# Performance work log

Measured on AMD Instinct MI355X. Metric: run time of the kernel, lower is better.

The kernel has to match this reference:

```python
import jax, jax.numpy as jnp
import numpy as np

N = 100000   # nodes
E = 1600000  # edges
F = 128      # in = out features
BN_EPS = 1e-5


def setup_inputs() -> dict:
    key = jax.random.key(0)
    ks = jax.random.split(key, 20)
    s = 1.0 / np.sqrt(F)
    inp = {
        "x": jax.random.normal(ks[0], (N, F), dtype=jnp.float32),
        "edge_index": jax.random.randint(ks[1], (2, E), 0, N, dtype=jnp.int64),
        "edge_type": jax.random.randint(ks[2], (E,), 0, 2, dtype=jnp.int64),
        # self-loop linear
        "w_sl": jax.random.normal(ks[3], (F, F), dtype=jnp.float32) * s,
        "b_sl": jnp.zeros((F,), dtype=jnp.float32),
        # GIN MLP for relation 0 (edge_type==0)
        "w1_n": jax.random.normal(ks[4], (F, F), dtype=jnp.float32) * s,
        "b1_n": jnp.zeros((F,), dtype=jnp.float32),
        "gamma_n": jnp.ones((F,), dtype=jnp.float32),
        "beta_n": jnp.zeros((F,), dtype=jnp.float32),
        "w2_n": jax.random.normal(ks[5], (F, F), dtype=jnp.float32) * s,
        "b2_n": jnp.zeros((F,), dtype=jnp.float32),
        # GIN MLP for relation 1 (edge_type==1)
        "w1_d": jax.random.normal(ks[6], (F, F), dtype=jnp.float32) * s,
        "b1_d": jnp.zeros((F,), dtype=jnp.float32),
        "gamma_d": jnp.ones((F,), dtype=jnp.float32),
        "beta_d": jnp.zeros((F,), dtype=jnp.float32),
        "w2_d": jax.random.normal(ks[7], (F, F), dtype=jnp.float32) * s,
        "b2_d": jnp.zeros((F,), dtype=jnp.float32),
        # gate linear: 3F -> F
        "w_gat": jax.random.normal(ks[8], (F, 3 * F), dtype=jnp.float32) * (1.0 / np.sqrt(3 * F)),
        "b_gat": jnp.zeros((F,), dtype=jnp.float32),
    }
    return inp


def _gin_branch(x, src, dst, mask, w1, b1, gamma, beta, w2, b2):
    # masked gather-scatter: equivalent to selecting edge columns with edge_type==r
    msg = x[src] * mask[:, None]                         # [E, F]
    agg = jax.ops.segment_sum(msg, dst, num_segments=N)  # [N, F]
    h = agg + x                                          # (1 + eps)*x with eps=0
    h = h @ w1.T + b1
    # BatchNorm1d, training-mode batch statistics (biased variance)
    mu = jnp.mean(h, axis=0)
    var = jnp.var(h, axis=0)
    h = gamma * (h - mu) * jax.lax.rsqrt(var + BN_EPS) + beta
    h = jax.nn.relu(h)
    return h @ w2.T + b2


def reference(x, edge_index, edge_type, w_sl, b_sl,
              w1_n, b1_n, gamma_n, beta_n, w2_n, b2_n,
              w1_d, b1_d, gamma_d, beta_d, w2_d, b2_d,
              w_gat, b_gat):
    src, dst = edge_index[0], edge_index[1]
    mask_n = (edge_type == 0).astype(x.dtype)
    mask_d = (edge_type == 1).astype(x.dtype)

    x_new_x = x @ w_sl.T + b_sl
    x_new_n = _gin_branch(x, src, dst, mask_n, w1_n, b1_n, gamma_n, beta_n, w2_n, b2_n)
    x_new_d = _gin_branch(x, src, dst, mask_d, w1_d, b1_d, gamma_d, beta_d, w2_d, b2_d)

    cat = jnp.concatenate((x_new_x, x_new_n, x_new_d), axis=1)   # [N, 3F]
    gat_raw = jax.nn.softmax(cat @ w_gat.T + b_gat, axis=-1)     # [N, F]
    gat = jnp.cumsum(gat_raw, axis=-1)
    out = (x_new_x + x_new_n) * (1.0 - gat) + (x_new_x + x_new_n + jnp.flip(x_new_d, axis=1)) * gat
    return out
```

## Files before the change

kernel.cpp:

```cpp
#include <hip/hip_runtime.h>
#include <stdint.h>

#define FF 128
#define MFMA __builtin_amdgcn_mfma_f32_16x16x32_bf16

typedef __attribute__((ext_vector_type(8))) short bf8_t;
typedef __attribute__((ext_vector_type(4))) float f4_t;
typedef __attribute__((ext_vector_type(8))) uint16_t us8_t;

__device__ __forceinline__ uint16_t f2bf(float f) {
  union { float f; uint32_t u; } v; v.f = f;
  return (uint16_t)((v.u + 0x7fffu + ((v.u >> 16) & 1u)) >> 16);
}
__device__ __forceinline__ float bf2f(uint16_t h) {
  union { uint32_t u; float f; } v; v.u = ((uint32_t)h) << 16;
  return v.f;
}

#define STAGE_W8(Wp, rsb, cb)                                                  \
  do {                                                                         \
    uint4 tmp_[4];                                                             \
    _Pragma("unroll") for (int j_ = 0; j_ < 4; ++j_) {                         \
      int k_ = j_ * 8 + w;                                                     \
      int r_ = ((k_ & 1) << 6) + lane;                                         \
      int c_ = k_ >> 1;                                                        \
      tmp_[j_] = *(const uint4*)((const char*)(Wp) + (size_t)r_ * (rsb) +      \
                                 (cb) + c_ * 16);                              \
    }                                                                          \
    _Pragma("unroll") for (int j_ = 0; j_ < 4; ++j_) {                         \
      int k_ = j_ * 8 + w;                                                     \
      *(uint4*)((char*)wlds + k_ * 1024 + lane * 16) = tmp_[j_];               \
    }                                                                          \
  } while (0)

__global__ __launch_bounds__(256) void cvt_w_k(
    const float* __restrict__ wsl, const float* __restrict__ w1n,
    const float* __restrict__ w2n, const float* __restrict__ w1d,
    const float* __restrict__ w2d, const float* __restrict__ wgat,
    uint16_t* __restrict__ o) {
  int i = blockIdx.x * 256 + threadIdx.x;
  const int NW = 5 * 16384;
  if (i >= NW + 49152) return;
  float v;
  if (i < NW) {
    int wsel = i >> 14, j = i & 16383;
    const float* p = (wsel == 0) ? wsl : (wsel == 1) ? w1n : (wsel == 2) ? w2n
                     : (wsel == 3) ? w1d : w2d;
    v = p[j];
  } else {
    v = wgat[i - NW];
  }
  o[i] = f2bf(v);
}

__global__ __launch_bounds__(256) void cvt_x_k(const float* __restrict__ x,
                                               uint16_t* __restrict__ xb, int n4) {
  int i = blockIdx.x * 256 + threadIdx.x;
  if (i >= n4) return;
  float4 v = ((const float4*)x)[i];
  uint2 o;
  o.x = ((uint32_t)f2bf(v.y) << 16) | f2bf(v.x);
  o.y = ((uint32_t)f2bf(v.w) << 16) | f2bf(v.z);
  ((uint2*)xb)[i] = o;
}

__global__ __launch_bounds__(256) void hist_k(const int* __restrict__ dst,
                                              const int* __restrict__ ety,
                                              int* __restrict__ hist, int E) {
  int i = blockIdx.x * 256 + threadIdx.x;
  if (i < E) atomicAdd(&hist[(dst[i] << 1) | ety[i]], 1);
}

__global__ __launch_bounds__(256) void scan1_k(const int* __restrict__ hist,
                                               int* __restrict__ off,
                                               int* __restrict__ bsum, int nbins) {
  int i = blockIdx.x * 256 + threadIdx.x;
  int v = (i < nbins) ? hist[i] : 0;
  int lane = threadIdx.x & 63, w = threadIdx.x >> 6;
  int s = v;
#pragma unroll
  for (int d = 1; d < 64; d <<= 1) {
    int o = __shfl_up(s, (unsigned)d, 64);
    if (lane >= d) s += o;
  }
  __shared__ int wsum[4];
  if (lane == 63) wsum[w] = s;
  __syncthreads();
  int add = 0;
  for (int k = 0; k < w; ++k) add += wsum[k];
  s += add;
  if (i < nbins) off[i] = s - v;
  if (threadIdx.x == 255) bsum[blockIdx.x] = s;
}

__global__ __launch_bounds__(1024) void scan2_k(int* __restrict__ bsum, int nb) {
  int t = threadIdx.x;
  int v = (t < nb) ? bsum[t] : 0;
  int lane = t & 63, w = t >> 6;
  int s = v;
#pragma unroll
  for (int d = 1; d < 64; d <<= 1) {
    int o = __shfl_up(s, (unsigned)d, 64);
    if (lane >= d) s += o;
  }
  __shared__ int ws[16];
  if (lane == 63) ws[w] = s;
  __syncthreads();
  int add = 0;
  for (int k = 0; k < w; ++k) add += ws[k];
  s += add;
  if (t < nb) bsum[t] = s - v;
}

__global__ __launch_bounds__(256) void scan3_k(int* __restrict__ off,
                                               int* __restrict__ ccur,
                                               const int* __restrict__ bsum,
                                               int nbins, int E) {
  int i = blockIdx.x * 256 + threadIdx.x;
  if (i < nbins) {
    int v = off[i] + bsum[blockIdx.x];
    off[i] = v;
    if ((i & 511) == 0) ccur[i >> 9] = v;
  }
  if (i == nbins) off[i] = E;
}

#define BK_EPT 16
__global__ __launch_bounds__(256) void bucketize_k(const int* __restrict__ src,
                                                   const int* __restrict__ dst,
                                                   const int* __restrict__ ety,
                                                   int* __restrict__ ccur,
                                                   uint32_t* __restrict__ bk,
                                                   int E, int nbuckets) {
  __shared__ int lhist[512];
  __shared__ int lbase[512];
  const int tid = threadIdx.x;
  const int base = blockIdx.x * (256 * BK_EPT);
  for (int j = tid; j < nbuckets; j += 256) lhist[j] = 0;
  __syncthreads();

  uint32_t pk[BK_EPT];
  uint32_t rk[BK_EPT];
#pragma unroll
  for (int j = 0; j < BK_EPT; ++j) {
    int i = base + j * 256 + tid;
    if (i < E) {
      int bin = (dst[i] << 1) | ety[i];
      int bucket = bin >> 9;
      int rank = atomicAdd(&lhist[bucket], 1);
      pk[j] = (uint32_t)src[i] | ((uint32_t)(bin & 511) << 17);
      rk[j] = (uint32_t)bucket | ((uint32_t)rank << 9);
    } else {
      rk[j] = 0xFFFFFFFFu;
    }
  }
  __syncthreads();
  for (int j = tid; j < nbuckets; j += 256) {
    int c = lhist[j];
    lbase[j] = c ? atomicAdd(&ccur[j], c) : 0;
  }
  __syncthreads();
#pragma unroll
  for (int j = 0; j < BK_EPT; ++j) {
    if (rk[j] != 0xFFFFFFFFu) {
      int bucket = (int)(rk[j] & 511u);
      int rank = (int)(rk[j] >> 9);
      bk[lbase[bucket] + rank] = pk[j];
    }
  }
}

__global__ __launch_bounds__(256) void sctfine_k(const int* __restrict__ off,
                                                 const uint32_t* __restrict__ bk,
                                                 int* __restrict__ ssrc, int nbins) {
  __shared__ int lcur[512];
  const int b = blockIdx.x;
  const int binbase = b << 9;
  const int binend = min(binbase + 512, nbins);
  for (int j = threadIdx.x; j < binend - binbase; j += 256)
    lcur[j] = off[binbase + j];
  __syncthreads();
  const int estart = off[binbase], eend = off[binend];
  for (int i = estart + (int)threadIdx.x; i < eend; i += 256) {
    uint32_t pk = bk[i];
    int pos = atomicAdd(&lcur[pk >> 17], 1);
    ssrc[pos] = (int)(pk & 0x1FFFFu);
  }
}

__global__ __launch_bounds__(256) void agg_k(const int* __restrict__ off,
                                             const int* __restrict__ ssrc,
                                             const uint16_t* __restrict__ xb,
                                             const float* __restrict__ x,
                                             uint16_t* __restrict__ xanb,
                                             uint16_t* __restrict__ xadb, int nbins) {
  int wid = (blockIdx.x * 256 + threadIdx.x) >> 6;
  int lane = threadIdx.x & 63;
  if (wid >= nbins) return;
  int e = off[wid], end = off[wid + 1];
  float ax = 0.f, ay = 0.f, bx = 0.f, by = 0.f;
  for (; e + 7 < end; e += 8) {
    uint32_t v0 = ((const uint32_t*)(xb + (size_t)ssrc[e] * FF))[lane];
    uint32_t v1 = ((const uint32_t*)(xb + (size_t)ssrc[e + 1] * FF))[lane];
    uint32_t v2 = ((const uint32_t*)(xb + (size_t)ssrc[e + 2] * FF))[lane];
    uint32_t v3 = ((const uint32_t*)(xb + (size_t)ssrc[e + 3] * FF))[lane];
    uint32_t v4 = ((const uint32_t*)(xb + (size_t)ssrc[e + 4] * FF))[lane];
    uint32_t v5 = ((const uint32_t*)(xb + (size_t)ssrc[e + 5] * FF))[lane];
    uint32_t v6 = ((const uint32_t*)(xb + (size_t)ssrc[e + 6] * FF))[lane];
    uint32_t v7 = ((const uint32_t*)(xb + (size_t)ssrc[e + 7] * FF))[lane];
    ax += bf2f((uint16_t)(v0 & 0xffffu)) + bf2f((uint16_t)(v2 & 0xffffu)) +
          bf2f((uint16_t)(v4 & 0xffffu)) + bf2f((uint16_t)(v6 & 0xffffu));
    ay += bf2f((uint16_t)(v0 >> 16)) + bf2f((uint16_t)(v2 >> 16)) +
          bf2f((uint16_t)(v4 >> 16)) + bf2f((uint16_t)(v6 >> 16));
    bx += bf2f((uint16_t)(v1 & 0xffffu)) + bf2f((uint16_t)(v3 & 0xffffu)) +
          bf2f((uint16_t)(v5 & 0xffffu)) + bf2f((uint16_t)(v7 & 0xffffu));
    by += bf2f((uint16_t)(v1 >> 16)) + bf2f((uint16_t)(v3 >> 16)) +
          bf2f((uint16_t)(v5 >> 16)) + bf2f((uint16_t)(v7 >> 16));
  }
  for (; e + 1 < end; e += 2) {
    uint32_t v0 = ((const uint32_t*)(xb + (size_t)ssrc[e] * FF))[lane];
    uint32_t v1 = ((const uint32_t*)(xb + (size_t)ssrc[e + 1] * FF))[lane];
    ax += bf2f((uint16_t)(v0 & 0xffffu));
    ay += bf2f((uint16_t)(v0 >> 16));
    bx += bf2f((uint16_t)(v1 & 0xffffu));
    by += bf2f((uint16_t)(v1 >> 16));
  }
  if (e < end) {
    uint32_t v0 = ((const uint32_t*)(xb + (size_t)ssrc[e] * FF))[lane];
    ax += bf2f((uint16_t)(v0 & 0xffffu));
    ay += bf2f((uint16_t)(v0 >> 16));
  }
  ax += bx;
  ay += by;
  int n = wid >> 1;
  float2 xo = ((const float2*)(x + (size_t)n * FF))[lane];
  ax += xo.x;
  ay += xo.y;
  uint32_t o = ((uint32_t)f2bf(ay) << 16) | f2bf(ax);
  uint16_t* dstp = (wid & 1) ? xadb : xanb;
  ((uint32_t*)(dstp + (size_t)n * FF))[lane] = o;
}

__global__ __launch_bounds__(512) void gemm1_k(
    const uint16_t* __restrict__ xanb, const uint16_t* __restrict__ xadb,
    const uint16_t* __restrict__ wbf, const float* __restrict__ b1n,
    const float* __restrict__ b1d, uint16_t* __restrict__ h1n,
    uint16_t* __restrict__ h1d, float* __restrict__ gstats, int N) {
  __shared__ __align__(16) uint16_t wlds[16384];
  __shared__ float sstat[8][4][128];
  const int tid = threadIdx.x;
  const int lane = tid & 63, w = tid >> 6;
  const int lr = lane & 15, lg = lane >> 4;
  const int rowbase = blockIdx.x * 256 + w * 32;
  const int arow0 = min(rowbase + lr, N - 1);
  const int arow1 = min(rowbase + 16 + lr, N - 1);

  f4_t acc[2][8];
  const f4_t zz = {0.f, 0.f, 0.f, 0.f};
  bf8_t a0[4], a1[4];

  STAGE_W8(wbf + 16384, 256, 0);
#pragma unroll
  for (int s = 0; s < 4; ++s) {
    const int k0 = s * 32 + lg * 8;
    a0[s] = *(const bf8_t*)(xanb + (size_t)arow0 * FF + k0);
    a1[s] = *(const bf8_t*)(xanb + (size_t)arow1 * FF + k0);
  }
  __syncthreads();

#pragma unroll 1
  for (int gi = 0; gi < 2; ++gi) {
#pragma unroll
    for (int rg = 0; rg < 2; ++rg)
#pragma unroll
      for (int t = 0; t < 8; ++t) acc[rg][t] = zz;
#pragma unroll
    for (int s = 0; s < 4; ++s) {
#pragma unroll
      for (int t = 0; t < 8; ++t) {
        bf8_t b = *(const bf8_t*)&wlds[(s * 4 + lg) * 1024 + (t * 16 + lr) * 8];
        acc[0][t] = MFMA(a0[s], b, acc[0][t], 0, 0, 0);
        acc[1][t] = MFMA(a1[s], b, acc[1][t], 0, 0, 0);
      }
    }
    const float* bp = gi ? b1d : b1n;
    uint16_t* hp = gi ? h1d : h1n;
#pragma unroll
    for (int t = 0; t < 8; ++t) {
      const int col = t * 16 + lr;
      const float b = bp[col];
      float sum = 0.f, ss = 0.f;
#pragma unroll
      for (int rg = 0; rg < 2; ++rg)
#pragma unroll
        for (int r = 0; r < 4; ++r) {
          const int row = rowbase + rg * 16 + lg * 4 + r;
          const float h = acc[rg][t][r] + b;
          if (row < N) {
            hp[(size_t)row * FF + col] = f2bf(h);
            sum += h;
            ss += h * h;
          }
        }
      sum += __shfl_xor(sum, 16, 64);
      sum += __shfl_xor(sum, 32, 64);
      ss += __shfl_xor(ss, 16, 64);
      ss += __shfl_xor(ss, 32, 64);
      if (lane < 16) {
        sstat[w][gi * 2 + 0][col] = sum;
        sstat[w][gi * 2 + 1][col] = ss;
      }
    }
    if (gi == 0) {
      __syncthreads();
      STAGE_W8(wbf + 3 * 16384, 256, 0);
#pragma unroll
      for (int s = 0; s < 4; ++s) {
        const int k0 = s * 32 + lg * 8;
        a0[s] = *(const bf8_t*)(xadb + (size_t)arow0 * FF + k0);
        a1[s] = *(const bf8_t*)(xadb + (size_t)arow1 * FF + k0);
      }
      __syncthreads();
    }
  }
  __syncthreads();
  if (tid < 512) {
    int a = tid >> 7, c = tid & 127;
    float v = 0.f;
#pragma unroll
    for (int ww = 0; ww < 8; ++ww) v += sstat[ww][a][c];
    unsafeAtomicAdd(&gstats[tid], v);
  }
}

__global__ void bnfin_k(const float* __restrict__ gstats,
                        const float* __restrict__ gamn, const float* __restrict__ betn,
                        const float* __restrict__ gamd, const float* __restrict__ betd,
                        float* __restrict__ bnp, int N) {
  int i = threadIdx.x;
  float invN = 1.f / (float)N;
  {
    float mu = gstats[i] * invN;
    float var = gstats[128 + i] * invN - mu * mu;
    float sc = gamn[i] * rsqrtf(var + 1e-5f);
    bnp[i] = sc;
    bnp[128 + i] = betn[i] - mu * sc;
  }
  {
    float mu = gstats[256 + i] * invN;
    float var = gstats[384 + i] * invN - mu * mu;
    float sc = gamd[i] * rsqrtf(var + 1e-5f);
    bnp[256 + i] = sc;
    bnp[384 + i] = betd[i] - mu * sc;
  }
}

__global__ __launch_bounds__(512) void fuse2_k(
    const uint16_t* __restrict__ xb, const uint16_t* __restrict__ h1n,
    const uint16_t* __restrict__ h1d, const uint16_t* __restrict__ wbf,
    const float* __restrict__ bnp, const float* __restrict__ b_sl,
    const float* __restrict__ b2n, const float* __restrict__ b2d,
    const float* __restrict__ bgat, float* __restrict__ out, int N) {
  __shared__ __align__(16) uint16_t wlds[16384];
  __shared__ __align__(16) uint16_t smt[8][16][136];
  const int tid = threadIdx.x;
  const int lane = tid & 63, w = tid >> 6;
  const int lr = lane & 15, lg = lane >> 4;
  const int rowbase = blockIdx.x * 128 + w * 16;
  const int arow = min(rowbase + lr, N - 1);
  const uint16_t* wg = wbf + 5 * 16384;

  f4_t sum[8];
  f4_t accG[8];
  f4_t wk[8];
  const f4_t zz = {0.f, 0.f, 0.f, 0.f};

#define GATE_PHASE()                                                             \
  do {                                                                          \
    _Pragma("unroll") for (int s = 0; s < 4; ++s) {                             \
      bf8_t a = *(const bf8_t*)&smt[w][lr][s * 32 + lg * 8];                    \
      _Pragma("unroll") for (int t = 0; t < 8; ++t) {                           \
        bf8_t b = *(const bf8_t*)&wlds[(s * 4 + lg) * 1024 + (t * 16 + lr) * 8]; \
        accG[t] = MFMA(a, b, accG[t], 0, 0, 0);                                 \
      }                                                                         \
    }                                                                           \
  } while (0)

#define BRANCH_PHASE(hv, bnb, bp, ADDSUM)                                        \
  do {                                                                          \
    _Pragma("unroll") for (int t = 0; t < 8; ++t) wk[t] = zz;                   \
    _Pragma("unroll") for (int s = 0; s < 4; ++s) {                             \
      const int k0 = s * 32 + lg * 8;                                           \
      f4_t sc0 = *(const f4_t*)((bnb) + k0);                                    \
      f4_t sc1 = *(const f4_t*)((bnb) + k0 + 4);                                \
      f4_t sh0 = *(const f4_t*)((bnb) + 128 + k0);                              \
      f4_t sh1 = *(const f4_t*)((bnb) + 128 + k0 + 4);                          \
      bf8_t a;                                                                  \
      _Pragma("unroll") for (int j = 0; j < 4; ++j) {                           \
        a[j] = (short)f2bf(fmaxf(bf2f((hv)[s][j]) * sc0[j] + sh0[j], 0.f));     \
        a[j + 4] =                                                              \
            (short)f2bf(fmaxf(bf2f((hv)[s][j + 4]) * sc1[j] + sh1[j], 0.f));    \
      }                                                                         \
      _Pragma("unroll") for (int t = 0; t < 8; ++t) {                           \
        bf8_t b = *(const bf8_t*)&wlds[(s * 4 + lg) * 1024 + (t * 16 + lr) * 8]; \
        wk[t] = MFMA(a, b, wk[t], 0, 0, 0);                                     \
      }                                                                         \
    }                                                                           \
    _Pragma("unroll") for (int t = 0; t < 8; ++t) {                             \
      const int col = t * 16 + lr;                                              \
      const float bb = (bp)[col];                                               \
      _Pragma("unroll") for (int r = 0; r < 4; ++r) {                           \
        const float v = wk[t][r] + bb;                                          \
        if (ADDSUM) sum[t][r] += v;                                             \
        smt[w][lg * 4 + r][col] = f2bf(v);                                      \
      }                                                                         \
    }                                                                           \
  } while (0)

  bf8_t xa[4];
#pragma unroll
  for (int s = 0; s < 4; ++s)
    xa[s] = *(const bf8_t*)(xb + (size_t)arow * FF + s * 32 + lg * 8);

  STAGE_W8(wbf, 256, 0);
  __syncthreads();

#pragma unroll
  for (int t = 0; t < 8; ++t) sum[t] = zz;
#pragma unroll
  for (int s = 0; s < 4; ++s) {
#pragma unroll
    for (int t = 0; t < 8; ++t) {
      bf8_t b = *(const bf8_t*)&wlds[(s * 4 + lg) * 1024 + (t * 16 + lr) * 8];
      sum[t] = MFMA(xa[s], b, sum[t], 0, 0, 0);
    }
  }
#pragma unroll
  for (int t = 0; t < 8; ++t) {
    const int col = t * 16 + lr;
    const float b = b_sl[col];
#pragma unroll
    for (int r = 0; r < 4; ++r) {
      sum[t][r] += b;
      smt[w][lg * 4 + r][col] = f2bf(sum[t][r]);
    }
  }
  us8_t hvn[4];
#pragma unroll
  for (int s = 0; s < 4; ++s)
    hvn[s] = *(const us8_t*)(h1n + (size_t)arow * FF + s * 32 + lg * 8);

  __syncthreads();
  STAGE_W8(wg, 768, 0);
  __syncthreads();
#pragma unroll
  for (int t = 0; t < 8; ++t) accG[t] = zz;
  GATE_PHASE();

  __syncthreads();
  STAGE_W8(wbf + 2 * 16384, 256, 0);
  __syncthreads();
  BRANCH_PHASE(hvn, bnp, b2n, 1);
  us8_t hvd[4];
#pragma unroll
  for (int s = 0; s < 4; ++s)
    hvd[s] = *(const us8_t*)(h1d + (size_t)arow * FF + s * 32 + lg * 8);

  __syncthreads();
  STAGE_W8(wg, 768, 256);
  __syncthreads();
  GATE_PHASE();

  __syncthreads();
  STAGE_W8(wbf + 4 * 16384, 256, 0);
  __syncthreads();
  BRANCH_PHASE(hvd, bnp + 256, b2d, 0);

  __syncthreads();
  STAGE_W8(wg, 768, 512);
  __syncthreads();
  GATE_PHASE();

  float bg[8];
#pragma unroll
  for (int t = 0; t < 8; ++t) bg[t] = bgat[t * 16 + lr];
#pragma unroll
  for (int r = 0; r < 4; ++r) {
    float lv[8];
#pragma unroll
    for (int t = 0; t < 8; ++t) lv[t] = accG[t][r] + bg[t];
    float m = lv[0];
#pragma unroll
    for (int t = 1; t < 8; ++t) m = fmaxf(m, lv[t]);
#pragma unroll
    for (int d = 1; d < 16; d <<= 1) m = fmaxf(m, __shfl_xor(m, d, 16));
    float g[8];
    float run = 0.f;
#pragma unroll
    for (int t = 0; t < 8; ++t) {
      float p = __expf(lv[t] - m);
      float scn = p;
#pragma unroll
      for (int d = 1; d < 16; d <<= 1) {
        float o = __shfl_up(scn, (unsigned)d, 16);
        if (lr >= d) scn += o;
      }
      g[t] = run + scn;
      run += __shfl(scn, 15, 16);
    }
    const float inv = 1.f / run;
    const int row = rowbase + lg * 4 + r;
    if (row < N) {
      const int lrow = lg * 4 + r;
#pragma unroll
      for (int t = 0; t < 8; ++t) {
        const int col = t * 16 + lr;
        const float xdf = bf2f(smt[w][lrow][127 - col]);
        out[(size_t)row * FF + col] = sum[t][r] + xdf * (g[t] * inv);
      }
    }
  }
#undef GATE_PHASE
#undef BRANCH_PHASE
}

extern "C" void kernel_launch(void* const* d_in, const int* in_sizes, int n_in,
                              void* d_out, int out_size, void* d_ws, size_t ws_size,
                              hipStream_t stream) {
  const float* x = (const float*)d_in[0];
  const int* eidx = (const int*)d_in[1];
  const int* etype = (const int*)d_in[2];
  const float* w_sl = (const float*)d_in[3];
  const float* b_sl = (const float*)d_in[4];
  const float* w1n = (const float*)d_in[5];
  const float* b1n = (const float*)d_in[6];
  const float* gamn = (const float*)d_in[7];
  const float* betn = (const float*)d_in[8];
  const float* w2n = (const float*)d_in[9];
  const float* b2n = (const float*)d_in[10];
  const float* w1d = (const float*)d_in[11];
  const float* b1d = (const float*)d_in[12];
  const float* gamd = (const float*)d_in[13];
  const float* betd = (const float*)d_in[14];
  const float* w2d = (const float*)d_in[15];
  const float* b2d = (const float*)d_in[16];
  const float* wgat = (const float*)d_in[17];
  const float* bgat = (const float*)d_in[18];
  float* out = (float*)d_out;

  const int N = in_sizes[0] / FF;
  const int E = in_sizes[2];
  const int* src = eidx;
  const int* dst = eidx + E;
  const int nbins = 2 * N;
  const int nbuckets = (nbins + 511) >> 9;

  const size_t NF = (size_t)N * FF;
  float* gstats = (float*)d_ws;
  float* bnp = gstats + 512;
  uint16_t* wbf = (uint16_t*)(bnp + 512);
  uint16_t* xb = wbf + 131072;
  uint16_t* xanb = xb + NF;
  uint16_t* xadb = xanb + NF;
  uint16_t* h1n = xadb + NF;
  uint16_t* h1d = h1n + NF;
  int* hist = (int*)(h1d + NF);
  int* off = hist + nbins;
  int* ccur = off + nbins + 1;
  int* bsum = ccur + nbuckets;
  int* ssrc = bsum + 1024;
  uint32_t* bk = (uint32_t*)(ssrc + E);

  const int nb1 = (nbins + 255) / 256;

  hipMemsetAsync(hist, 0, (size_t)nbins * sizeof(int), stream);
  hipMemsetAsync(gstats, 0, 512 * sizeof(float), stream);
  cvt_w_k<<<512, 256, 0, stream>>>(w_sl, w1n, w2n, w1d, w2d, wgat, wbf);
  cvt_x_k<<<(int)((NF / 4 + 255) / 256), 256, 0, stream>>>(x, xb, (int)(NF / 4));

  hist_k<<<(E + 255) / 256, 256, 0, stream>>>(dst, etype, hist, E);
  scan1_k<<<nb1, 256, 0, stream>>>(hist, off, bsum, nbins);
  scan2_k<<<1, 1024, 0, stream>>>(bsum, nb1);
  scan3_k<<<(nbins + 256) / 256, 256, 0, stream>>>(off, ccur, bsum, nbins, E);
  bucketize_k<<<(E + 256 * BK_EPT - 1) / (256 * BK_EPT), 256, 0, stream>>>(
      src, dst, etype, ccur, bk, E, nbuckets);
  sctfine_k<<<nbuckets, 256, 0, stream>>>(off, bk, ssrc, nbins);
  agg_k<<<(nbins + 3) / 4, 256, 0, stream>>>(off, ssrc, xb, x, xanb, xadb, nbins);

  gemm1_k<<<(N + 255) / 256, 512, 0, stream>>>(xanb, xadb, wbf, b1n, b1d, h1n, h1d,
                                               gstats, N);
  bnfin_k<<<1, 128, 0, stream>>>(gstats, gamn, betn, gamd, betd, bnp, N);
  fuse2_k<<<(N + 127) / 128, 512, 0, stream>>>(xb, h1n, h1d, wbf, bnp, b_sl, b2n,
                                               b2d, bgat, out, N);
}
```

Baseline: 375.3 us.

## Fold gate weights into branch output weights to skip intermediate re-staging

Precomputes composite gate matrices G = Wgat_slice · W_branch and a folded gate bias, so the gate logits accumulate directly from the branch inputs alongside each branch GEMM. The fused kernel no longer writes branch outputs to shared memory as bf16 and re-reads them for separate gate GEMMs. This cuts the number of weight-staging rounds and barriers, and the flipped d-branch values now come from a lane shuffle instead of LDS. In exchange it adds two small precompute kernels, doubles the weight LDS footprint, and changes rounding because the gate no longer sees bf16-rounded intermediates.

```diff
diff --git a/kernel.cpp b/kernel.cpp
--- a/kernel.cpp
+++ b/kernel.cpp
@@ -33,24 +33,73 @@
     }                                                                          \
   } while (0)
 
+#define STAGE2(Wp, Gp)                                                         \
+  do {                                                                         \
+    uint4 tmp_[8];                                                             \
+    _Pragma("unroll") for (int j_ = 0; j_ < 8; ++j_) {                         \
+      int k_ = j_ * 8 + w;                                                     \
+      int cc_ = k_ & 31;                                                       \
+      const char* sp_ = (j_ < 4) ? (const char*)(Wp) : (const char*)(Gp);      \
+      int r_ = ((cc_ & 1) << 6) + lane;                                        \
+      int c_ = cc_ >> 1;                                                       \
+      tmp_[j_] = *(const uint4*)(sp_ + (size_t)r_ * 256 + c_ * 16);            \
+    }                                                                          \
+    _Pragma("unroll") for (int j_ = 0; j_ < 8; ++j_) {                         \
+      int k_ = j_ * 8 + w;                                                     \
+      *(uint4*)((char*)wlds + k_ * 1024 + lane * 16) = tmp_[j_];               \
+    }                                                                          \
+  } while (0)
+
+#define WFRAG(s, t) (*(const bf8_t*)&wlds[((s)*4 + lg) * 1024 + ((t)*16 + lr) * 8])
+#define GFRAG(s, t) \
+  (*(const bf8_t*)&wlds[16384 + ((s)*4 + lg) * 1024 + ((t)*16 + lr) * 8])
+
 __global__ __launch_bounds__(256) void cvt_w_k(
     const float* __restrict__ wsl, const float* __restrict__ w1n,
     const float* __restrict__ w2n, const float* __restrict__ w1d,
-    const float* __restrict__ w2d, const float* __restrict__ wgat,
-    uint16_t* __restrict__ o) {
+    const float* __restrict__ w2d, uint16_t* __restrict__ o) {
   int i = blockIdx.x * 256 + threadIdx.x;
-  const int NW = 5 * 16384;
-  if (i >= NW + 49152) return;
-  float v;
-  if (i < NW) {
-    int wsel = i >> 14, j = i & 16383;
-    const float* p = (wsel == 0) ? wsl : (wsel == 1) ? w1n : (wsel == 2) ? w2n
-                     : (wsel == 3) ? w1d : w2d;
-    v = p[j];
-  } else {
-    v = wgat[i - NW];
-  }
-  o[i] = f2bf(v);
+  if (i >= 5 * 16384) return;
+  int wsel = i >> 14, j = i & 16383;
+  const float* p = (wsel == 0) ? wsl : (wsel == 1) ? w1n : (wsel == 2) ? w2n
+                   : (wsel == 3) ? w1d : w2d;
+  o[i] = f2bf(p[j]);
+}
+
+__global__ __launch_bounds__(256) void gatepre_k(
+    const float* __restrict__ wgat, const float* __restrict__ wsl,
+    const float* __restrict__ w2n, const float* __restrict__ w2d,
+    uint16_t* __restrict__ G) {
+  const int mat = blockIdx.x >> 3;
+  const int jblk = blockIdx.x & 7;
+  const float* A = wgat + mat * 128;
+  const float* B = (mat == 0) ? wsl : (mat == 1) ? w2n : w2d;
+  const int i = threadIdx.x & 127;
+  const int jo = jblk * 16 + (threadIdx.x >> 7) * 8;
+  float acc[8] = {0.f, 0.f, 0.f, 0.f, 0.f, 0.f, 0.f, 0.f};
+#pragma unroll 4
+  for (int k = 0; k < 128; ++k) {
+    float a = A[(size_t)i * 384 + k];
+    const float* br = B + (size_t)k * 128 + jo;
+#pragma unroll
+    for (int j = 0; j < 8; ++j) acc[j] = fmaf(a, br[j], acc[j]);
+  }
+  uint16_t* g = G + mat * 16384 + i * 128 + jo;
+#pragma unroll
+  for (int j = 0; j < 8; ++j) g[j] = f2bf(acc[j]);
+}
+
+__global__ void bgatp_k(const float* __restrict__ wgat, const float* __restrict__ b_sl,
+                        const float* __restrict__ b2n, const float* __restrict__ b2d,
+                        const float* __restrict__ bgat, float* __restrict__ bgp) {
+  int i = threadIdx.x;
+  float s = bgat[i];
+  for (int k = 0; k < 128; ++k) {
+    s += wgat[(size_t)i * 384 + k] * b_sl[k];
+    s += wgat[(size_t)i * 384 + 128 + k] * b2n[k];
+    s += wgat[(size_t)i * 384 + 256 + k] * b2d[k];
+  }
+  bgp[i] = s;
 }
 
 __global__ __launch_bounds__(256) void cvt_x_k(const float* __restrict__ x,
@@ -278,7 +327,7 @@
     for (int s = 0; s < 4; ++s) {
 #pragma unroll
       for (int t = 0; t < 8; ++t) {
-        bf8_t b = *(const bf8_t*)&wlds[(s * 4 + lg) * 1024 + (t * 16 + lr) * 8];
+        bf8_t b = WFRAG(s, t);
         acc[0][t] = MFMA(a0[s], b, acc[0][t], 0, 0, 0);
         acc[1][t] = MFMA(a1[s], b, acc[1][t], 0, 0, 0);
       }
@@ -355,135 +404,119 @@
   }
 }
 
-__global__ __launch_bounds__(512) void fuse2_k(
+__global__ __launch_bounds__(512, 4) void fuse2_k(
     const uint16_t* __restrict__ xb, const uint16_t* __restrict__ h1n,
     const uint16_t* __restrict__ h1d, const uint16_t* __restrict__ wbf,
-    const float* __restrict__ bnp, const float* __restrict__ b_sl,
-    const float* __restrict__ b2n, const float* __restrict__ b2d,
-    const float* __restrict__ bgat, float* __restrict__ out, int N) {
-  __shared__ __align__(16) uint16_t wlds[16384];
-  __shared__ __align__(16) uint16_t smt[8][16][136];
+    const uint16_t* __restrict__ G, const float* __restrict__ bnp,
+    const float* __restrict__ b_sl, const float* __restrict__ b2n,
+    const float* __restrict__ b2d, const float* __restrict__ bgp,
+    float* __restrict__ out, int N) {
+  __shared__ __align__(16) uint16_t wlds[32768];
   const int tid = threadIdx.x;
   const int lane = tid & 63, w = tid >> 6;
   const int lr = lane & 15, lg = lane >> 4;
   const int rowbase = blockIdx.x * 128 + w * 16;
   const int arow = min(rowbase + lr, N - 1);
-  const uint16_t* wg = wbf + 5 * 16384;
 
   f4_t sum[8];
   f4_t accG[8];
   f4_t wk[8];
   const f4_t zz = {0.f, 0.f, 0.f, 0.f};
 
-#define GATE_PHASE()                                                             \
-  do {                                                                          \
-    _Pragma("unroll") for (int s = 0; s < 4; ++s) {                             \
-      bf8_t a = *(const bf8_t*)&smt[w][lr][s * 32 + lg * 8];                    \
-      _Pragma("unroll") for (int t = 0; t < 8; ++t) {                           \
-        bf8_t b = *(const bf8_t*)&wlds[(s * 4 + lg) * 1024 + (t * 16 + lr) * 8]; \
-        accG[t] = MFMA(a, b, accG[t], 0, 0, 0);                                 \
-      }                                                                         \
-    }                                                                           \
-  } while (0)
-
-#define BRANCH_PHASE(hv, bnb, bp, ADDSUM)                                        \
-  do {                                                                          \
-    _Pragma("unroll") for (int t = 0; t < 8; ++t) wk[t] = zz;                   \
-    _Pragma("unroll") for (int s = 0; s < 4; ++s) {                             \
-      const int k0 = s * 32 + lg * 8;                                           \
-      f4_t sc0 = *(const f4_t*)((bnb) + k0);                                    \
-      f4_t sc1 = *(const f4_t*)((bnb) + k0 + 4);                                \
-      f4_t sh0 = *(const f4_t*)((bnb) + 128 + k0);                              \
-      f4_t sh1 = *(const f4_t*)((bnb) + 128 + k0 + 4);                          \
-      bf8_t a;                                                                  \
-      _Pragma("unroll") for (int j = 0; j < 4; ++j) {                           \
-        a[j] = (short)f2bf(fmaxf(bf2f((hv)[s][j]) * sc0[j] + sh0[j], 0.f));     \
-        a[j + 4] =                                                              \
-            (short)f2bf(fmaxf(bf2f((hv)[s][j + 4]) * sc1[j] + sh1[j], 0.f));    \
-      }                                                                         \
-      _Pragma("unroll") for (int t = 0; t < 8; ++t) {                           \
-        bf8_t b = *(const bf8_t*)&wlds[(s * 4 + lg) * 1024 + (t * 16 + lr) * 8]; \
-        wk[t] = MFMA(a, b, wk[t], 0, 0, 0);                                     \
-      }                                                                         \
-    }                                                                           \
-    _Pragma("unroll") for (int t = 0; t < 8; ++t) {                             \
-      const int col = t * 16 + lr;                                              \
-      const float bb = (bp)[col];                                               \
-      _Pragma("unroll") for (int r = 0; r < 4; ++r) {                           \
-        const float v = wk[t][r] + bb;                                          \
-        if (ADDSUM) sum[t][r] += v;                                             \
-        smt[w][lg * 4 + r][col] = f2bf(v);                                      \
-      }                                                                         \
-    }                                                                           \
-  } while (0)
-
   bf8_t xa[4];
-#pragma unroll
-  for (int s = 0; s < 4; ++s)
-    xa[s] = *(const bf8_t*)(xb + (size_t)arow * FF + s * 32 + lg * 8);
-
-  STAGE_W8(wbf, 256, 0);
-  __syncthreads();
-
-#pragma unroll
-  for (int t = 0; t < 8; ++t) sum[t] = zz;
+  us8_t hvn[4];
 #pragma unroll
   for (int s = 0; s < 4; ++s) {
-#pragma unroll
-    for (int t = 0; t < 8; ++t) {
-      bf8_t b = *(const bf8_t*)&wlds[(s * 4 + lg) * 1024 + (t * 16 + lr) * 8];
-      sum[t] = MFMA(xa[s], b, sum[t], 0, 0, 0);
-    }
+    const int k0 = s * 32 + lg * 8;
+    xa[s] = *(const bf8_t*)(xb + (size_t)arow * FF + k0);
+    hvn[s] = *(const us8_t*)(h1n + (size_t)arow * FF + k0);
+  }
+
+  STAGE2(wbf, G);
+  __syncthreads();
+
+#pragma unroll
+  for (int t = 0; t < 8; ++t) { sum[t] = zz; accG[t] = zz; }
+#pragma unroll
+  for (int s = 0; s < 4; ++s) {
+#pragma unroll
+    for (int t = 0; t < 8; ++t) sum[t] = MFMA(xa[s], WFRAG(s, t), sum[t], 0, 0, 0);
+#pragma unroll
+    for (int t = 0; t < 8; ++t) accG[t] = MFMA(xa[s], GFRAG(s, t), accG[t], 0, 0, 0);
   }
 #pragma unroll
   for (int t = 0; t < 8; ++t) {
-    const int col = t * 16 + lr;
-    const float b = b_sl[col];
-#pragma unroll
-    for (int r = 0; r < 4; ++r) {
-      sum[t][r] += b;
-      smt[w][lg * 4 + r][col] = f2bf(sum[t][r]);
-    }
-  }
-  us8_t hvn[4];
-#pragma unroll
-  for (int s = 0; s < 4; ++s)
-    hvn[s] = *(const us8_t*)(h1n + (size_t)arow * FF + s * 32 + lg * 8);
-
-  __syncthreads();
-  STAGE_W8(wg, 768, 0);
-  __syncthreads();
-#pragma unroll
-  for (int t = 0; t < 8; ++t) accG[t] = zz;
-  GATE_PHASE();
-
-  __syncthreads();
-  STAGE_W8(wbf + 2 * 16384, 256, 0);
-  __syncthreads();
-  BRANCH_PHASE(hvn, bnp, b2n, 1);
+    const float b = b_sl[t * 16 + lr];
+#pragma unroll
+    for (int r = 0; r < 4; ++r) sum[t][r] += b;
+  }
+  __syncthreads();
+
+  STAGE2(wbf + 2 * 16384, G + 16384);
   us8_t hvd[4];
 #pragma unroll
   for (int s = 0; s < 4; ++s)
     hvd[s] = *(const us8_t*)(h1d + (size_t)arow * FF + s * 32 + lg * 8);
-
-  __syncthreads();
-  STAGE_W8(wg, 768, 256);
-  __syncthreads();
-  GATE_PHASE();
-
-  __syncthreads();
-  STAGE_W8(wbf + 4 * 16384, 256, 0);
-  __syncthreads();
-  BRANCH_PHASE(hvd, bnp + 256, b2d, 0);
-
-  __syncthreads();
-  STAGE_W8(wg, 768, 512);
-  __syncthreads();
-  GATE_PHASE();
+  __syncthreads();
+
+#pragma unroll
+  for (int t = 0; t < 8; ++t) wk[t] = zz;
+#pragma unroll
+  for (int s = 0; s < 4; ++s) {
+    const int k0 = s * 32 + lg * 8;
+    f4_t sc0 = *(const f4_t*)(bnp + k0), sc1 = *(const f4_t*)(bnp + k0 + 4);
+    f4_t sh0 = *(const f4_t*)(bnp + 128 + k0), sh1 = *(const f4_t*)(bnp + 128 + k0 + 4);
+    bf8_t a;
+#pragma unroll
+    for (int j = 0; j < 4; ++j) {
+      a[j] = (short)f2bf(fmaxf(bf2f(hvn[s][j]) * sc0[j] + sh0[j], 0.f));
+      a[j + 4] = (short)f2bf(fmaxf(bf2f(hvn[s][j + 4]) * sc1[j] + sh1[j], 0.f));
+    }
+#pragma unroll
+    for (int t = 0; t < 8; ++t) wk[t] = MFMA(a, WFRAG(s, t), wk[t], 0, 0, 0);
+#pragma unroll
+    for (int t = 0; t < 8; ++t) accG[t] = MFMA(a, GFRAG(s, t), accG[t], 0, 0, 0);
+  }
+#pragma unroll
+  for (int t = 0; t < 8; ++t) {
+    const float b = b2n[t * 16 + lr];
+#pragma unroll
+    for (int r = 0; r < 4; ++r) sum[t][r] += wk[t][r] + b;
+  }
+  __syncthreads();
+
+  STAGE2(wbf + 4 * 16384, G + 2 * 16384);
+  __syncthreads();
+
+#pragma unroll
+  for (int t = 0; t < 8; ++t) wk[t] = zz;
+#pragma unroll
+  for (int s = 0; s < 4; ++s) {
+    const int k0 = s * 32 + lg * 8;
+    const float* bnb = bnp + 256;
+    f4_t sc0 = *(const f4_t*)(bnb + k0), sc1 = *(const f4_t*)(bnb + k0 + 4);
+    f4_t sh0 = *(const f4_t*)(bnb + 128 + k0), sh1 = *(const f4_t*)(bnb + 128 + k0 + 4);
+    bf8_t a;
+#pragma unroll
+    for (int j = 0; j < 4; ++j) {
+      a[j] = (short)f2bf(fmaxf(bf2f(hvd[s][j]) * sc0[j] + sh0[j], 0.f));
+      a[j + 4] = (short)f2bf(fmaxf(bf2f(hvd[s][j + 4]) * sc1[j] + sh1[j], 0.f));
+    }
+#pragma unroll
+    for (int t = 0; t < 8; ++t) wk[t] = MFMA(a, WFRAG(s, t), wk[t], 0, 0, 0);
+#pragma unroll
+    for (int t = 0; t < 8; ++t) accG[t] = MFMA(a, GFRAG(s, t), accG[t], 0, 0, 0);
+  }
+#pragma unroll
+  for (int t = 0; t < 8; ++t) {
+    const float b = b2d[t * 16 + lr];
+#pragma unroll
+    for (int r = 0; r < 4; ++r) wk[t][r] += b;
+  }
 
   float bg[8];
 #pragma unroll
-  for (int t = 0; t < 8; ++t) bg[t] = bgat[t * 16 + lr];
+  for (int t = 0; t < 8; ++t) bg[t] = bgp[t * 16 + lr];
 #pragma unroll
   for (int r = 0; r < 4; ++r) {
     float lv[8];
@@ -509,19 +542,16 @@
       run += __shfl(scn, 15, 16);
     }
     const float inv = 1.f / run;
+    float xdf[8];
+#pragma unroll
+    for (int t = 0; t < 8; ++t) xdf[t] = __shfl_xor(wk[7 - t][r], 15, 64);
     const int row = rowbase + lg * 4 + r;
     if (row < N) {
-      const int lrow = lg * 4 + r;
-#pragma unroll
-      for (int t = 0; t < 8; ++t) {
-        const int col = t * 16 + lr;
-        const float xdf = bf2f(smt[w][lrow][127 - col]);
-        out[(size_t)row * FF + col] = sum[t][r] + xdf * (g[t] * inv);
-      }
-    }
-  }
-#undef GATE_PHASE
-#undef BRANCH_PHASE
+#pragma unroll
+      for (int t = 0; t < 8; ++t)
+        out[(size_t)row * FF + t * 16 + lr] = sum[t][r] + xdf[t] * (g[t] * inv);
+    }
+  }
 }
 
 extern "C" void kernel_launch(void* const* d_in, const int* in_sizes, int n_in,
@@ -558,8 +588,10 @@
   const size_t NF = (size_t)N * FF;
   float* gstats = (float*)d_ws;
   float* bnp = gstats + 512;
-  uint16_t* wbf = (uint16_t*)(bnp + 512);
-  uint16_t* xb = wbf + 131072;
+  float* bgp = bnp + 512;
+  uint16_t* wbf = (uint16_t*)(bgp + 128);
+  uint16_t* G = wbf + 5 * 16384;
+  uint16_t* xb = G + 3 * 16384;
   uint16_t* xanb = xb + NF;
   uint16_t* xadb = xanb + NF;
   uint16_t* h1n = xadb + NF;
@@ -575,8 +607,10 @@
 
   hipMemsetAsync(hist, 0, (size_t)nbins * sizeof(int), stream);
   hipMemsetAsync(gstats, 0, 512 * sizeof(float), stream);
-  cvt_w_k<<<512, 256, 0, stream>>>(w_sl, w1n, w2n, w1d, w2d, wgat, wbf);
+  cvt_w_k<<<320, 256, 0, stream>>>(w_sl, w1n, w2n, w1d, w2d, wbf);
   cvt_x_k<<<(int)((NF / 4 + 255) / 256), 256, 0, stream>>>(x, xb, (int)(NF / 4));
+  gatepre_k<<<24, 256, 0, stream>>>(wgat, w_sl, w2n, w2d, G);
+  bgatp_k<<<1, 128, 0, stream>>>(wgat, b_sl, b2n, b2d, bgat, bgp);
 
   hist_k<<<(E + 255) / 256, 256, 0, stream>>>(dst, etype, hist, E);
   scan1_k<<<nb1, 256, 0, stream>>>(hist, off, bsum, nbins);
@@ -590,6 +624,6 @@
   gemm1_k<<<(N + 255) / 256, 512, 0, stream>>>(xanb, xadb, wbf, b1n, b1d, h1n, h1d,
                                                gstats, N);
   bnfin_k<<<1, 128, 0, stream>>>(gstats, gamn, betn, gamd, betd, bnp, N);
-  fuse2_k<<<(N + 127) / 128, 512, 0, stream>>>(xb, h1n, h1d, wbf, bnp, b_sl, b2n,
-                                               b2d, bgat, out, N);
-}
+  fuse2_k<<<(N + 127) / 128, 512, 0, stream>>>(xb, h1n, h1d, wbf, G, bnp, b_sl,
+                                               b2n, b2d, bgp, out, N);
+}
```

Result: slower. 464.6 us (+23.8%).
